# Performance work log

Hardware: AMD Instinct MI355X
Metric: run time of the kernel (lower is better)

The kernel has to match this reference:

```python
import jax, jax.numpy as jnp
import numpy as np

EPS_DIV = 1e-7   # matches .div(sigma + 1e-07) and denominator + 1e-07
EPS_NORM = 1e-12  # torch F.normalize default eps


def setup_inputs() -> dict:
    key = jax.random.key(0)
    k1, k2, k3, k4 = jax.random.split(key, 4)
    B, C, H, W = 4, 128, 64, 64
    K = 32
    stdv = 1.0 / np.sqrt(C)
    return {
        "x": jax.random.normal(k1, (B, C, H, W), dtype=jnp.float32),
        "anchor": jax.random.uniform(k2, (K, C), dtype=jnp.float32),
        "sigma_param": jax.random.uniform(k3, (K, C), dtype=jnp.float32),
        "gcn_weight": jax.random.uniform(k4, (C, C), dtype=jnp.float32,
                                         minval=-stdv, maxval=stdv),
    }


def _l2_normalize(v, axis):
    n = jnp.sqrt(jnp.sum(v * v, axis=axis, keepdims=True))
    return v / jnp.maximum(n, EPS_NORM)


def reference(x, anchor, sigma_param, gcn_weight):
    B, C, H, W = x.shape
    N = H * W
    K = anchor.shape[0]

    # --- GraphNet (NetVLAD-style soft assignment pooling) ---
    sigma = jax.nn.sigmoid(sigma_param)                        # [K, C]
    xf = x.reshape(B, C, N).transpose(0, 2, 1)                 # [B, N, C]
    # residual: [B, K, N, C]
    residual = (xf[:, None, :, :] - anchor[None, :, None, :]) / (
        sigma[None, :, None, :] + EPS_DIV)
    logits = -0.5 * jnp.sum(residual * residual, axis=3)       # [B, K, N]
    soft_assign = jax.nn.softmax(logits, axis=1)               # softmax over nodes K

    numerator = jnp.einsum('bknc,bkn->bkc', residual, soft_assign)  # [B, K, C]
    denominator = jnp.sum(soft_assign, axis=2)[..., None]           # [B, K, 1]
    nodes = numerator / (denominator + EPS_DIV)                     # [B, K, C]

    nodes = _l2_normalize(nodes, axis=2)
    flat = nodes.reshape(B, -1)
    flat = _l2_normalize(flat, axis=1)
    graph = flat.reshape(B, C, K)  # note: pure reshape as in torch .view

    # --- CascadeGCNet, loop = 1 ---
    adj = jnp.einsum('bck,bcl->bkl', graph, graph)             # x_t @ x -> [B, K, K]
    adj = jax.nn.softmax(adj, axis=2)
    support = jnp.einsum('bck,cd->bkd', graph, gcn_weight)     # [B, K, C]
    graph = jnp.einsum('bkl,bld->bkd', adj, support).transpose(0, 2, 1)  # [B, C, K]
    graph = jax.nn.relu(graph)

    # --- project back ---
    out = jnp.einsum('bck,bkn->bcn', graph, soft_assign)       # [B, C, N]
    return out.reshape(B, C, H, W)
```

## Files before the change

### kernel.cpp

```cpp
#include <hip/hip_runtime.h>
#include <math.h>

#define BB 4
#define CC 128
#define KK 32
#define NN 4096
#define NSL 64

__device__ inline float bcastf(float v, int l) {
  return __uint_as_float(__builtin_amdgcn_readlane(__float_as_uint(v), (unsigned)l));
}

__launch_bounds__(512)
__global__ void k_A(const float* __restrict__ x, const float* __restrict__ anchor,
                    const float* __restrict__ sigp, float* __restrict__ sa,
                    float* __restrict__ pnum, float* __restrict__ pden) {
  const int b  = blockIdx.y, s = blockIdx.x;
  const int n0 = s * 64;
  const int t  = threadIdx.x;
  const int lane = t & 63;
  const int w  = __builtin_amdgcn_readfirstlane(t >> 6);

  __shared__ float xt[CC][68];
  __shared__ float lgT[64][40];
  __shared__ float stK[KK][68];
  __shared__ float pdenP[8][36];

  {
    const int ct = t >> 4, pt = t & 15;
    const float* xb = x + (size_t)b * CC * NN + n0 + 4 * pt;
#pragma unroll
    for (int pass = 0; pass < 4; pass++) {
      int c = ct + pass * 32;
      float4 v = *(const float4*)(xb + (size_t)c * NN);
      *(float4*)&xt[c][4 * pt] = v;
    }
  }

  float w2a[4], awa[4], w2b[4], awb[4];
  float ck0, ck1, ck2, ck3;
  {
    float cks[4];
#pragma unroll
    for (int i = 0; i < 4; i++) {
      const int k = 4 * w + i;
      float spa = sigp[k * CC + lane];
      float spb = sigp[k * CC + 64 + lane];
      float aa  = anchor[k * CC + lane];
      float ab  = anchor[k * CC + 64 + lane];
      float s1  = 1.0f / (1.0f + expf(-spa));
      float s2  = 1.0f / (1.0f + expf(-spb));
      float iva = 1.0f / (s1 + 1e-7f);
      float ivb = 1.0f / (s2 + 1e-7f);
      w2a[i] = iva * iva;            w2b[i] = ivb * ivb;
      awa[i] = -2.0f * aa * w2a[i];  awb[i] = -2.0f * ab * w2b[i];
      cks[i] = aa * aa * w2a[i] + ab * ab * w2b[i];
    }
#pragma unroll
    for (int d = 1; d < 64; d <<= 1) {
      cks[0] += __shfl_xor(cks[0], d);
      cks[1] += __shfl_xor(cks[1], d);
      cks[2] += __shfl_xor(cks[2], d);
      cks[3] += __shfl_xor(cks[3], d);
    }
    ck0 = cks[0]; ck1 = cks[1]; ck2 = cks[2]; ck3 = cks[3];
  }
  __syncthreads();

  {
    float a0 = 0.f, a1 = 0.f, a2 = 0.f, a3 = 0.f;
    for (int c = 0; c < 64; c++) {
      float xv = xt[c][lane];
      float x2 = xv * xv;
      a0 = fmaf(x2, bcastf(w2a[0], c), fmaf(xv, bcastf(awa[0], c), a0));
      a1 = fmaf(x2, bcastf(w2a[1], c), fmaf(xv, bcastf(awa[1], c), a1));
      a2 = fmaf(x2, bcastf(w2a[2], c), fmaf(xv, bcastf(awa[2], c), a2));
      a3 = fmaf(x2, bcastf(w2a[3], c), fmaf(xv, bcastf(awa[3], c), a3));
    }
    for (int c = 0; c < 64; c++) {
      float xv = xt[64 + c][lane];
      float x2 = xv * xv;
      a0 = fmaf(x2, bcastf(w2b[0], c), fmaf(xv, bcastf(awb[0], c), a0));
      a1 = fmaf(x2, bcastf(w2b[1], c), fmaf(xv, bcastf(awb[1], c), a1));
      a2 = fmaf(x2, bcastf(w2b[2], c), fmaf(xv, bcastf(awb[2], c), a2));
      a3 = fmaf(x2, bcastf(w2b[3], c), fmaf(xv, bcastf(awb[3], c), a3));
    }
    float4 lg;
    lg.x = -0.5f * (a0 + ck0);
    lg.y = -0.5f * (a1 + ck1);
    lg.z = -0.5f * (a2 + ck2);
    lg.w = -0.5f * (a3 + ck3);
    *(float4*)&lgT[lane][w * 4] = lg;
  }
  __syncthreads();

  {
    const int p  = w * 8 + (lane >> 3);
    const int kq = lane & 7;
    float4 lv = *(float4*)&lgT[p][kq * 4];
    float m = fmaxf(fmaxf(lv.x, lv.y), fmaxf(lv.z, lv.w));
    m = fmaxf(m, __shfl_xor(m, 1));
    m = fmaxf(m, __shfl_xor(m, 2));
    m = fmaxf(m, __shfl_xor(m, 4));
    float e0 = __expf(lv.x - m), e1 = __expf(lv.y - m);
    float e2 = __expf(lv.z - m), e3 = __expf(lv.w - m);
    float sum = e0 + e1 + e2 + e3;
    sum += __shfl_xor(sum, 1);
    sum += __shfl_xor(sum, 2);
    sum += __shfl_xor(sum, 4);
    float rs = 1.0f / sum;
    e0 *= rs; e1 *= rs; e2 *= rs; e3 *= rs;
    stK[kq * 4 + 0][p] = e0;
    stK[kq * 4 + 1][p] = e1;
    stK[kq * 4 + 2][p] = e2;
    stK[kq * 4 + 3][p] = e3;
    float p0 = e0, p1 = e1, p2 = e2, p3 = e3;
    p0 += __shfl_xor(p0, 8);  p1 += __shfl_xor(p1, 8);
    p2 += __shfl_xor(p2, 8);  p3 += __shfl_xor(p3, 8);
    p0 += __shfl_xor(p0, 16); p1 += __shfl_xor(p1, 16);
    p2 += __shfl_xor(p2, 16); p3 += __shfl_xor(p3, 16);
    p0 += __shfl_xor(p0, 32); p1 += __shfl_xor(p1, 32);
    p2 += __shfl_xor(p2, 32); p3 += __shfl_xor(p3, 32);
    if (lane < 8) {
      pdenP[w][lane * 4 + 0] = p0;
      pdenP[w][lane * 4 + 1] = p1;
      pdenP[w][lane * 4 + 2] = p2;
      pdenP[w][lane * 4 + 3] = p3;
    }
  }
  __syncthreads();

  if (t < KK) {
    float d = 0.f;
#pragma unroll
    for (int ww = 0; ww < 8; ww++) d += pdenP[ww][t];
    pden[((size_t)b * NSL + s) * KK + t] = d;
  }

  {
    const int k = t >> 4, j4 = t & 15;
    float4 v = *(float4*)&stK[k][4 * j4];
    *(float4*)(sa + ((size_t)b * KK + k) * NN + n0 + 4 * j4) = v;
  }

  {
    const int k = t & 31, cg = t >> 5;
    float acc[8];
#pragma unroll
    for (int i = 0; i < 8; i++) acc[i] = 0.f;
    const float* xb = x + (size_t)(b * CC + cg * 8) * NN + n0;
    for (int j4 = 0; j4 < 16; j4++) {
      float4 sv = *(float4*)&stK[k][4 * j4];
#pragma unroll
      for (int i = 0; i < 8; i++) {
        float4 xr = *(const float4*)(xb + (size_t)i * NN + 4 * j4);
        acc[i] = fmaf(sv.x, xr.x, acc[i]);
        acc[i] = fmaf(sv.y, xr.y, acc[i]);
        acc[i] = fmaf(sv.z, xr.z, acc[i]);
        acc[i] = fmaf(sv.w, xr.w, acc[i]);
      }
    }
    float* pp = pnum + (((size_t)b * NSL + s) * KK + k) * CC + cg * 8;
    *(float4*)pp       = make_float4(acc[0], acc[1], acc[2], acc[3]);
    *(float4*)(pp + 4) = make_float4(acc[4], acc[5], acc[6], acc[7]);
  }
}

__launch_bounds__(256)
__global__ void k_red(const float* __restrict__ pnum, const float* __restrict__ pden,
                      const float* __restrict__ sigp, const float* __restrict__ anchor,
                      float* __restrict__ nodes, float* __restrict__ n1sq) {
  const int t = threadIdx.x;
  const int g = blockIdx.x * 256 + t;
  const int c = g & 127, k = (g >> 7) & 31, b = g >> 12;

  float dk = 0.0f;
#pragma unroll 8
  for (int s = 0; s < NSL; s++) dk += pden[((size_t)b * NSL + s) * KK + k];

  float q = 0.0f;
#pragma unroll 8
  for (int s = 0; s < NSL; s++)
    q += pnum[(((size_t)b * NSL + s) * KK + k) * CC + c];

  const int idx = k * CC + c;
  float sg = 1.0f / (1.0f + expf(-sigp[idx]));
  float iv = 1.0f / (sg + 1e-7f);
  float val = iv * (q - anchor[idx] * dk) / (dk + 1e-7f);
  nodes[((size_t)b * KK + k) * CC + c] = val;

  __shared__ float red[256];
  red[t] = val * val;
  __syncthreads();
  for (int sft = 64; sft > 0; sft >>= 1) {
    if ((t & 127) < sft) red[t] += red[t + sft];
    __syncthreads();
  }
  if ((t & 127) == 0) n1sq[b * KK + k] = red[t];
}

__launch_bounds__(1024)
__global__ void k_gcn2(const float* __restrict__ nodes, const float* __restrict__ n1sq,
                       const float* __restrict__ W, float* __restrict__ GB) {
  const int b = blockIdx.x;
  const int t = threadIdx.x;
  __shared__ float flat[KK * CC];
  __shared__ float sup[KK][130];
  __shared__ float adjm[KK][33];
  __shared__ float n1v[KK], nsq[KK];
  __shared__ float n2s;

  const int k = t >> 5, cq = t & 31;
  float4 val = ((const float4*)(nodes + (size_t)b * KK * CC))[k * 32 + cq];

  if (t < KK) {
    float s2 = n1sq[b * KK + t];
    float n1 = fmaxf(sqrtf(s2), 1e-12f);
    n1v[t] = n1;
    nsq[t] = s2 / (n1 * n1);
  }
  __syncthreads();
  if (t == 0) {
    float tot = 0.0f;
#pragma unroll
    for (int kk = 0; kk < KK; kk++) tot += nsq[kk];
    n2s = fmaxf(sqrtf(tot), 1e-12f);
  }
  __syncthreads();
  {
    float sc = 1.0f / (n1v[k] * n2s);
    val.x *= sc; val.y *= sc; val.z *= sc; val.w *= sc;
    ((float4*)flat)[k * 32 + cq] = val;
  }
  __syncthreads();

  {
    const int k2 = t >> 5, l = t & 31;
    float a = 0.0f;
#pragma unroll 8
    for (int i = 0; i < CC; i++)
      a = fmaf(flat[i * KK + k2], flat[i * KK + l], a);
    adjm[k2][l] = a;
  }
  __syncthreads();
  if (t < KK) {
    float m = -1e30f;
#pragma unroll
    for (int l = 0; l < KK; l++) m = fmaxf(m, adjm[t][l]);
    float s2 = 0.0f;
#pragma unroll
    for (int l = 0; l < KK; l++) { float e = __expf(adjm[t][l] - m); adjm[t][l] = e; s2 += e; }
    float r = 1.0f / s2;
#pragma unroll
    for (int l = 0; l < KK; l++) adjm[t][l] *= r;
  }
  __syncthreads();

  const int d = t & 127, lg = t >> 7;
  float sacc[4] = {0.0f, 0.0f, 0.0f, 0.0f};
  for (int c = 0; c < CC; c++) {
    float wv = W[c * CC + d];
#pragma unroll
    for (int j = 0; j < 4; j++)
      sacc[j] = fmaf(flat[c * KK + lg + 8 * j], wv, sacc[j]);
  }
#pragma unroll
  for (int j = 0; j < 4; j++) sup[lg + 8 * j][d] = sacc[j];
  __syncthreads();

#pragma unroll
  for (int j = 0; j < 4; j++) {
    int kk = lg + 8 * j;
    float g = 0.0f;
#pragma unroll
    for (int l = 0; l < KK; l++) g = fmaf(adjm[kk][l], sup[l][d], g);
    GB[((size_t)b * CC + d) * KK + kk] = fmaxf(g, 0.0f);
  }
}

__launch_bounds__(256)
__global__ void k_proj(const float* __restrict__ GB, const float* __restrict__ sa,
                       float* __restrict__ out) {
  const int b  = blockIdx.y;
  const int n0 = blockIdx.x * 64;
  const int t  = threadIdx.x;
  const int nl = t & 63;
  const int cg = __builtin_amdgcn_readfirstlane(t >> 6);

  float sreg[KK];
  const float* spt = sa + (size_t)b * KK * NN + n0 + nl;
#pragma unroll
  for (int k = 0; k < KK; k++) sreg[k] = spt[(size_t)k * NN];

  const float* gp = GB + ((size_t)b * CC + (size_t)cg * 32) * KK;
  float* op = out + ((size_t)b * CC + (size_t)cg * 32) * NN + n0 + nl;
#pragma unroll 2
  for (int ci = 0; ci < 32; ci++) {
    float acc = 0.0f;
#pragma unroll
    for (int k = 0; k < KK; k++) acc = fmaf(gp[ci * KK + k], sreg[k], acc);
    op[(size_t)ci * NN] = acc;
  }
}

extern "C" void kernel_launch(void* const* d_in, const int* in_sizes, int n_in,
                              void* d_out, int out_size, void* d_ws, size_t ws_size,
                              hipStream_t stream) {
  const float* x      = (const float*)d_in[0];
  const float* anchor = (const float*)d_in[1];
  const float* sigp   = (const float*)d_in[2];
  const float* W      = (const float*)d_in[3];
  float* out = (float*)d_out;

  float* ws    = (float*)d_ws;
  float* pden  = ws;
  float* pnum  = ws + 8192;
  float* nodes = ws + 1056768;
  float* n1sq  = ws + 1073152;
  float* GB    = ws + 1073280;
  float* sa    = ws + 1089664;

  k_A   <<<dim3(NSL, BB),     dim3(512),  0, stream>>>(x, anchor, sigp, sa, pnum, pden);
  k_red <<<dim3(64),          dim3(256),  0, stream>>>(pnum, pden, sigp, anchor, nodes, n1sq);
  k_gcn2<<<dim3(BB),          dim3(1024), 0, stream>>>(nodes, n1sq, W, GB);
  k_proj<<<dim3(NN / 64, BB), dim3(256),  0, stream>>>(GB, sa, out);
}
```

Measured before the change: 65.61 us.

## Register-tile logits computation with LDS-staged weights instead of readlane broadcasts

Replaces the per-wave readlane broadcast of per-channel weights with float4 weight tiles staged in shared memory. Each thread now computes a 4-pixel by 2-node register tile of logits over half the channels. The two channel halves are combined through a shared partial buffer. Anchor norm constants are reduced through shared memory instead of wave shuffles. This removes the scalar readlane bottleneck and raises FMA reuse per LDS load, at the cost of more shared memory and an extra reduction step.

```diff
diff --git a/kernel.cpp b/kernel.cpp
--- a/kernel.cpp
+++ b/kernel.cpp
@@ -6,10 +6,6 @@
 #define KK 32
 #define NN 4096
 #define NSL 64
-
-__device__ inline float bcastf(float v, int l) {
-  return __uint_as_float(__builtin_amdgcn_readlane(__float_as_uint(v), (unsigned)l));
-}
 
 __launch_bounds__(512)
 __global__ void k_A(const float* __restrict__ x, const float* __restrict__ anchor,
@@ -21,10 +17,13 @@
   const int lane = t & 63;
   const int w  = __builtin_amdgcn_readfirstlane(t >> 6);
 
-  __shared__ float xt[CC][68];
-  __shared__ float lgT[64][40];
-  __shared__ float stK[KK][68];
-  __shared__ float pdenP[8][36];
+  __shared__ float  xt[CC][68];
+  __shared__ float4 wt4[16][129];
+  __shared__ float  plg[2][64][36];
+  __shared__ float  stK[KK][68];
+  __shared__ float  ckp[KK][33];
+  __shared__ float  ckL[KK];
+  __shared__ float  pdenP[8][36];
 
   {
     const int ct = t >> 4, pt = t & 15;
@@ -37,67 +36,73 @@
     }
   }
 
-  float w2a[4], awa[4], w2b[4], awb[4];
-  float ck0, ck1, ck2, ck3;
-  {
-    float cks[4];
+  {
+    const int base = t * 4;
+    const int kp = base >> 7;
+    const int k0 = kp * 2, k1 = kp * 2 + 1;
+    float s0 = 0.f, s1 = 0.f;
+#pragma unroll
+    for (int e = 0; e < 4; e++) {
+      int c = (base + e) & 127;
+      float sp0 = sigp[k0 * CC + c], sp1 = sigp[k1 * CC + c];
+      float a0  = anchor[k0 * CC + c], a1 = anchor[k1 * CC + c];
+      float sg0 = 1.0f / (1.0f + expf(-sp0));
+      float sg1 = 1.0f / (1.0f + expf(-sp1));
+      float iv0 = 1.0f / (sg0 + 1e-7f), iv1 = 1.0f / (sg1 + 1e-7f);
+      float w20 = iv0 * iv0, w21 = iv1 * iv1;
+      wt4[kp][c] = make_float4(w20, -2.0f * a0 * w20, w21, -2.0f * a1 * w21);
+      s0 = fmaf(a0 * a0, w20, s0);
+      s1 = fmaf(a1 * a1, w21, s1);
+    }
+    ckp[k0][t & 31] = s0;
+    ckp[k1][t & 31] = s1;
+  }
+  __syncthreads();
+
+  if (t < KK) {
+    float ssum = 0.f;
+#pragma unroll
+    for (int j = 0; j < 32; j++) ssum += ckp[t][j];
+    ckL[t] = ssum;
+  }
+
+  {
+    const int px4 = t & 15, kp = (t >> 4) & 15, ch = t >> 8;
+    float acc[8];
+#pragma unroll
+    for (int i = 0; i < 8; i++) acc[i] = 0.f;
+    for (int c0 = 0; c0 < 64; c0++) {
+      const int c = ch * 64 + c0;
+      float4 xv = *(const float4*)&xt[c][px4 * 4];
+      float4 wv = wt4[kp][c];
+      acc[0] = fmaf(xv.x, fmaf(xv.x, wv.x, wv.y), acc[0]);
+      acc[1] = fmaf(xv.x, fmaf(xv.x, wv.z, wv.w), acc[1]);
+      acc[2] = fmaf(xv.y, fmaf(xv.y, wv.x, wv.y), acc[2]);
+      acc[3] = fmaf(xv.y, fmaf(xv.y, wv.z, wv.w), acc[3]);
+      acc[4] = fmaf(xv.z, fmaf(xv.z, wv.x, wv.y), acc[4]);
+      acc[5] = fmaf(xv.z, fmaf(xv.z, wv.z, wv.w), acc[5]);
+      acc[6] = fmaf(xv.w, fmaf(xv.w, wv.x, wv.y), acc[6]);
+      acc[7] = fmaf(xv.w, fmaf(xv.w, wv.z, wv.w), acc[7]);
+    }
 #pragma unroll
     for (int i = 0; i < 4; i++) {
-      const int k = 4 * w + i;
-      float spa = sigp[k * CC + lane];
-      float spb = sigp[k * CC + 64 + lane];
-      float aa  = anchor[k * CC + lane];
-      float ab  = anchor[k * CC + 64 + lane];
-      float s1  = 1.0f / (1.0f + expf(-spa));
-      float s2  = 1.0f / (1.0f + expf(-spb));
-      float iva = 1.0f / (s1 + 1e-7f);
-      float ivb = 1.0f / (s2 + 1e-7f);
-      w2a[i] = iva * iva;            w2b[i] = ivb * ivb;
-      awa[i] = -2.0f * aa * w2a[i];  awb[i] = -2.0f * ab * w2b[i];
-      cks[i] = aa * aa * w2a[i] + ab * ab * w2b[i];
-    }
-#pragma unroll
-    for (int d = 1; d < 64; d <<= 1) {
-      cks[0] += __shfl_xor(cks[0], d);
-      cks[1] += __shfl_xor(cks[1], d);
-      cks[2] += __shfl_xor(cks[2], d);
-      cks[3] += __shfl_xor(cks[3], d);
-    }
-    ck0 = cks[0]; ck1 = cks[1]; ck2 = cks[2]; ck3 = cks[3];
-  }
-  __syncthreads();
-
-  {
-    float a0 = 0.f, a1 = 0.f, a2 = 0.f, a3 = 0.f;
-    for (int c = 0; c < 64; c++) {
-      float xv = xt[c][lane];
-      float x2 = xv * xv;
-      a0 = fmaf(x2, bcastf(w2a[0], c), fmaf(xv, bcastf(awa[0], c), a0));
-      a1 = fmaf(x2, bcastf(w2a[1], c), fmaf(xv, bcastf(awa[1], c), a1));
-      a2 = fmaf(x2, bcastf(w2a[2], c), fmaf(xv, bcastf(awa[2], c), a2));
-      a3 = fmaf(x2, bcastf(w2a[3], c), fmaf(xv, bcastf(awa[3], c), a3));
-    }
-    for (int c = 0; c < 64; c++) {
-      float xv = xt[64 + c][lane];
-      float x2 = xv * xv;
-      a0 = fmaf(x2, bcastf(w2b[0], c), fmaf(xv, bcastf(awb[0], c), a0));
-      a1 = fmaf(x2, bcastf(w2b[1], c), fmaf(xv, bcastf(awb[1], c), a1));
-      a2 = fmaf(x2, bcastf(w2b[2], c), fmaf(xv, bcastf(awb[2], c), a2));
-      a3 = fmaf(x2, bcastf(w2b[3], c), fmaf(xv, bcastf(awb[3], c), a3));
-    }
-    float4 lg;
-    lg.x = -0.5f * (a0 + ck0);
-    lg.y = -0.5f * (a1 + ck1);
-    lg.z = -0.5f * (a2 + ck2);
-    lg.w = -0.5f * (a3 + ck3);
-    *(float4*)&lgT[lane][w * 4] = lg;
+      plg[ch][px4 * 4 + i][kp * 2 + 0] = acc[i * 2 + 0];
+      plg[ch][px4 * 4 + i][kp * 2 + 1] = acc[i * 2 + 1];
+    }
   }
   __syncthreads();
 
   {
     const int p  = w * 8 + (lane >> 3);
     const int kq = lane & 7;
-    float4 lv = *(float4*)&lgT[p][kq * 4];
+    float4 l0  = *(float4*)&plg[0][p][kq * 4];
+    float4 l1  = *(float4*)&plg[1][p][kq * 4];
+    float4 ckv = *(float4*)&ckL[kq * 4];
+    float4 lv;
+    lv.x = -0.5f * (l0.x + l1.x + ckv.x);
+    lv.y = -0.5f * (l0.y + l1.y + ckv.y);
+    lv.z = -0.5f * (l0.z + l1.z + ckv.z);
+    lv.w = -0.5f * (l0.w + l1.w + ckv.w);
     float m = fmaxf(fmaxf(lv.x, lv.y), fmaxf(lv.z, lv.w));
     m = fmaxf(m, __shfl_xor(m, 1));
     m = fmaxf(m, __shfl_xor(m, 2));
```

Result: faster. 59.42 us (-9.4%).
